# Kernel optimization log

Measured on AMD Instinct MI355X. Metric: run time of the kernel, lower is better.

## Reference

```python
import jax, jax.numpy as jnp
import numpy as np

B, N, E, H, HEADS = 4, 10000, 160000, 128, 4
NEG_SLOPE = 0.2  # PyG GATConv default
LN_EPS = 1e-5


def setup_inputs() -> dict:
    key = jax.random.key(0)
    ks = jax.random.split(key, 24)
    inp = {}
    inp["node_embeddings"] = jax.random.normal(ks[0], (B, N, H), dtype=jnp.float32)
    inp["src_index"] = jax.random.randint(ks[1], (B, E), 0, N)
    inp["tgt_index"] = jax.random.randint(ks[2], (B, E), 0, N)
    sc = 1.0 / np.sqrt(H)
    for i in range(3):
        j = 3 + 3 * i
        inp[f"W{i+1}"] = jax.random.normal(ks[j], (H, HEADS * H), dtype=jnp.float32) * sc
        inp[f"att_src{i+1}"] = jax.random.normal(ks[j + 1], (HEADS, H), dtype=jnp.float32) * sc
        inp[f"att_dst{i+1}"] = jax.random.normal(ks[j + 2], (HEADS, H), dtype=jnp.float32) * sc
        inp[f"bias{i+1}"] = jnp.zeros((H,), dtype=jnp.float32)
    inp["ln1_g"] = jnp.ones((H,), dtype=jnp.float32)
    inp["ln1_b"] = jnp.zeros((H,), dtype=jnp.float32)
    inp["ln2_g"] = jnp.ones((H,), dtype=jnp.float32)
    inp["ln2_b"] = jnp.zeros((H,), dtype=jnp.float32)
    return inp


def _layer_norm(x, g, b):
    mu = jnp.mean(x, axis=-1, keepdims=True)
    var = jnp.mean((x - mu) ** 2, axis=-1, keepdims=True)
    return (x - mu) * jax.lax.rsqrt(var + LN_EPS) * g + b


def _gat(x, src, tgt, W, a_s, a_d, b):
    # x: [N, H]; src/tgt: [E'] (self-loops already appended). eval mode -> no dropout.
    h = (x @ W).reshape(N, HEADS, H)               # [N, heads, H]
    e_src = jnp.einsum('nhc,hc->nh', h, a_s)       # [N, heads]
    e_dst = jnp.einsum('nhc,hc->nh', h, a_d)
    e = jax.nn.leaky_relu(e_src[src] + e_dst[tgt], NEG_SLOPE)  # [E', heads]
    m = jax.ops.segment_max(e, tgt, num_segments=N)            # per-target max
    ex = jnp.exp(e - m[tgt])
    s = jax.ops.segment_sum(ex, tgt, num_segments=N)
    alpha = ex / s[tgt]                                        # [E', heads]
    out = jax.ops.segment_sum(alpha[:, :, None] * h[src], tgt, num_segments=N)
    return out.mean(axis=1) + b                                # concat=False -> head mean


def reference(node_embeddings, src_index, tgt_index,
              W1, att_src1, att_dst1, bias1,
              W2, att_src2, att_dst2, bias2,
              W3, att_src3, att_dst3, bias3,
              ln1_g, ln1_b, ln2_g, ln2_b):
    loop = jnp.arange(N, dtype=src_index.dtype)

    def one_graph(x, src, tgt):
        s = jnp.concatenate([src, loop])   # GATConv add_self_loops=True (default)
        t = jnp.concatenate([tgt, loop])
        m = _gat(x, s, t, W1, att_src1, att_dst1, bias1)
        m = jax.nn.relu(_layer_norm(m, ln1_g, ln1_b))
        m = _gat(m, s, t, W2, att_src2, att_dst2, bias2)
        m = jax.nn.relu(_layer_norm(m, ln2_g, ln2_b))
        m = _gat(m, s, t, W3, att_src3, att_dst3, bias3)
        return m

    return jax.vmap(one_graph)(node_embeddings, src_index, tgt_index)
```

## Files before the change

kernel.cpp:

```cpp
#include <hip/hip_runtime.h>
#include <hip/hip_bf16.h>
#include <cstdint>
#include <cstddef>

#define B_ 4
#define N_ 10000
#define E_ 160000
#define H_ 128
#define HEADS_ 4
#define HH_ 512
#define NROWS (B_*N_)

typedef __attribute__((ext_vector_type(8))) short bf16x8;
typedef __attribute__((ext_vector_type(4))) float f32x4;

__device__ __forceinline__ float lrelu(float x){ return x > 0.f ? x : 0.2f*x; }
__device__ __forceinline__ unsigned short f2b(float f){
  unsigned int u = __builtin_bit_cast(unsigned int, f);
  unsigned int r = (u + 0x7fffu + ((u >> 16) & 1u)) >> 16;
  return (unsigned short)r;
}
__device__ __forceinline__ float blo(unsigned int u){ return __builtin_bit_cast(float, u << 16); }
__device__ __forceinline__ float bhi(unsigned int u){ return __builtin_bit_cast(float, u & 0xffff0000u); }

__global__ void k_count(const int* __restrict__ tgt, int* __restrict__ cnt){
  int e = blockIdx.x*blockDim.x + threadIdx.x;
  int b = blockIdx.y;
  int t = tgt[(size_t)b*E_ + e];
  atomicAdd(&cnt[b*N_ + t], 1);
}

__global__ void k_scan(const int* __restrict__ cnt, int* __restrict__ off, int* __restrict__ cursor){
  int b = blockIdx.x;
  __shared__ int wsum[16];
  __shared__ int carry_s;
  int lane = threadIdx.x & 63, wid = threadIdx.x >> 6;
  if (threadIdx.x == 0){ carry_s = 0; off[b*(N_+1)] = 0; }
  __syncthreads();
  for (int base = 0; base < N_; base += 1024){
    int i = base + threadIdx.x;
    int v = (i < N_) ? cnt[b*N_ + i] : 0;
    int x = v;
    #pragma unroll
    for (int d = 1; d < 64; d <<= 1){
      int y = __shfl_up(x, d);
      if (lane >= d) x += y;
    }
    if (lane == 63) wsum[wid] = x;
    __syncthreads();
    if (wid == 0 && lane < 16){
      int w = wsum[lane];
      #pragma unroll
      for (int d = 1; d < 16; d <<= 1){
        int y = __shfl_up(w, d, 16);
        if (lane >= d) w += y;
      }
      wsum[lane] = w;
    }
    __syncthreads();
    int excl = (wid ? wsum[wid-1] : 0) + carry_s;
    if (i < N_){
      int inc = x + excl;
      off[b*(N_+1) + i + 1] = inc;
      cursor[b*N_ + i] = inc - v;
    }
    __syncthreads();
    if (threadIdx.x == 0) carry_s += wsum[15];
    __syncthreads();
  }
}

__global__ void k_scatter(const int* __restrict__ src, const int* __restrict__ tgt,
                          int* __restrict__ cursor, int* __restrict__ csr){
  int e = blockIdx.x*blockDim.x + threadIdx.x;
  int b = blockIdx.y;
  int t = tgt[(size_t)b*E_ + e];
  int pos = atomicAdd(&cursor[b*N_ + t], 1);
  csr[(size_t)b*E_ + pos] = src[(size_t)b*E_ + e];
}

__global__ void k_wa(const float* __restrict__ W, const float* __restrict__ as_,
                     const float* __restrict__ ad_, float* __restrict__ was, float* __restrict__ wad){
  int i = blockIdx.x*blockDim.x + threadIdx.x;
  if (i >= H_*HEADS_) return;
  int k = i >> 2, h = i & 3;
  const float* wrow = W + (size_t)k*HH_ + h*H_;
  const float* asr = as_ + h*H_;
  const float* adr = ad_ + h*H_;
  float ss = 0.f, sd = 0.f;
  for (int c = 0; c < H_; ++c){ float w = wrow[c]; ss += w*asr[c]; sd += w*adr[c]; }
  was[i] = ss; wad[i] = sd;
}

__global__ void k_wprep(const float* __restrict__ W, unsigned short* __restrict__ Wt){
  int i = blockIdx.x*blockDim.x + threadIdx.x;
  int c = i >> 7, k = i & 127;
  Wt[i] = f2b(W[(size_t)k*HH_ + c]);
}

__global__ __launch_bounds__(256) void k_cast(const float* __restrict__ X, unsigned short* __restrict__ Xb){
  int i = blockIdx.x*blockDim.x + threadIdx.x;
  float4 v = ((const float4*)X)[i];
  ushort4 o; o.x = f2b(v.x); o.y = f2b(v.y); o.z = f2b(v.z); o.w = f2b(v.w);
  ((ushort4*)Xb)[i] = o;
}

__global__ __launch_bounds__(256) void k_logits(const unsigned short* __restrict__ Xb,
    const float* __restrict__ was, const float* __restrict__ wad,
    float* __restrict__ es, float* __restrict__ ed){
  int gw = (blockIdx.x * blockDim.x + threadIdx.x) >> 6;
  int lane = threadIdx.x & 63;
  unsigned int u = *(const unsigned int*)(Xb + (size_t)gw*H_ + lane*2);
  float xlo = blo(u), xhi = bhi(u);
  float4 w0 = *(const float4*)(was + lane*8);
  float4 w1 = *(const float4*)(was + lane*8 + 4);
  float4 d0 = *(const float4*)(wad + lane*8);
  float4 d1 = *(const float4*)(wad + lane*8 + 4);
  float s0 = xlo*w0.x + xhi*w1.x;
  float s1 = xlo*w0.y + xhi*w1.y;
  float s2 = xlo*w0.z + xhi*w1.z;
  float s3 = xlo*w0.w + xhi*w1.w;
  float t0 = xlo*d0.x + xhi*d1.x;
  float t1 = xlo*d0.y + xhi*d1.y;
  float t2 = xlo*d0.z + xhi*d1.z;
  float t3 = xlo*d0.w + xhi*d1.w;
  #pragma unroll
  for (int d = 1; d < 64; d <<= 1){
    s0 += __shfl_xor(s0, d); s1 += __shfl_xor(s1, d);
    s2 += __shfl_xor(s2, d); s3 += __shfl_xor(s3, d);
    t0 += __shfl_xor(t0, d); t1 += __shfl_xor(t1, d);
    t2 += __shfl_xor(t2, d); t3 += __shfl_xor(t3, d);
  }
  if (lane == 0){
    *(float4*)(es + (size_t)gw*4) = make_float4(s0, s1, s2, s3);
    *(float4*)(ed + (size_t)gw*4) = make_float4(t0, t1, t2, t3);
  }
}

__global__ __launch_bounds__(256) void k_gemm_mfma(const unsigned short* __restrict__ Xb,
    const unsigned short* __restrict__ Wt, unsigned short* __restrict__ Hb){
  __shared__ unsigned short xs[64*128];
  __shared__ unsigned short ws[64*128];
  int row0 = blockIdx.x * 64, col0 = blockIdx.y * 64;
  int tid = threadIdx.x;
  int ch = tid & 15, r0 = tid >> 4;
  #pragma unroll
  for (int p = 0; p < 4; ++p){
    int r = r0 + p*16;
    int sc = ch ^ (r & 7);
    *(uint4*)(&xs[r*128 + sc*8]) = *(const uint4*)(Xb + (size_t)(row0 + r)*H_ + ch*8);
    *(uint4*)(&ws[r*128 + sc*8]) = *(const uint4*)(Wt + (size_t)(col0 + r)*H_ + ch*8);
  }
  __syncthreads();
  int w = tid >> 6, l = tid & 63;
  int lr = l & 15, q = l >> 4;
  f32x4 z = {0.f, 0.f, 0.f, 0.f};
  f32x4 acc[4] = {z, z, z, z};
  int arow = w*16 + lr;
  #pragma unroll
  for (int kf = 0; kf < 4; ++kf){
    int bch = kf*4 + q;
    bf16x8 a = *(const bf16x8*)(&xs[arow*128 + (bch ^ (arow & 7))*8]);
    #pragma unroll
    for (int cf = 0; cf < 4; ++cf){
      int brow = cf*16 + lr;
      bf16x8 bfr = *(const bf16x8*)(&ws[brow*128 + (bch ^ (brow & 7))*8]);
      acc[cf] = __builtin_amdgcn_mfma_f32_16x16x32_bf16(a, bfr, acc[cf], 0, 0, 0);
    }
  }
  #pragma unroll
  for (int cf = 0; cf < 4; ++cf){
    #pragma unroll
    for (int rg = 0; rg < 4; ++rg){
      int row = row0 + w*16 + q*4 + rg;
      int col = col0 + cf*16 + lr;
      Hb[(size_t)row*HH_ + col] = f2b(acc[cf][rg]);
    }
  }
}

__global__ __launch_bounds__(256) void k_aggregate(const unsigned short* __restrict__ Hb,
    const float* __restrict__ es, const float* __restrict__ ed,
    const int* __restrict__ off, const int* __restrict__ csr,
    const float* __restrict__ bias, float* __restrict__ Y){
  int gw = (blockIdx.x * blockDim.x + threadIdx.x) >> 6;
  int lane = threadIdx.x & 63;
  int b = gw / N_;
  int t = gw - b*N_;
  const float4 edv = *(const float4*)(ed + (size_t)gw*4);
  int start = off[b*(N_+1) + t];
  int deg = off[b*(N_+1) + t + 1] - start;
  const int* lst = csr + (size_t)b*E_ + start;

  float m0=-1e30f, m1=-1e30f, m2=-1e30f, m3=-1e30f;
  float s0=0.f, s1=0.f, s2=0.f, s3=0.f;
  for (int i = lane; i <= deg; i += 64){
    int srcn = (i < deg) ? lst[i] : t;
    float4 ev = *(const float4*)(es + (size_t)(b*N_ + srcn)*4);
    float e0 = lrelu(ev.x + edv.x);
    float e1 = lrelu(ev.y + edv.y);
    float e2 = lrelu(ev.z + edv.z);
    float e3 = lrelu(ev.w + edv.w);
    float nm;
    nm = fmaxf(m0, e0); s0 = s0*__expf(m0-nm) + __expf(e0-nm); m0 = nm;
    nm = fmaxf(m1, e1); s1 = s1*__expf(m1-nm) + __expf(e1-nm); m1 = nm;
    nm = fmaxf(m2, e2); s2 = s2*__expf(m2-nm) + __expf(e2-nm); m2 = nm;
    nm = fmaxf(m3, e3); s3 = s3*__expf(m3-nm) + __expf(e3-nm); m3 = nm;
  }
  #pragma unroll
  for (int d = 1; d < 64; d <<= 1){
    float om, os, nm;
    om = __shfl_xor(m0, d); os = __shfl_xor(s0, d); nm = fmaxf(m0, om);
    s0 = s0*__expf(m0-nm) + os*__expf(om-nm); m0 = nm;
    om = __shfl_xor(m1, d); os = __shfl_xor(s1, d); nm = fmaxf(m1, om);
    s1 = s1*__expf(m1-nm) + os*__expf(om-nm); m1 = nm;
    om = __shfl_xor(m2, d); os = __shfl_xor(s2, d); nm = fmaxf(m2, om);
    s2 = s2*__expf(m2-nm) + os*__expf(om-nm); m2 = nm;
    om = __shfl_xor(m3, d); os = __shfl_xor(s3, d); nm = fmaxf(m3, om);
    s3 = s3*__expf(m3-nm) + os*__expf(om-nm); m3 = nm;
  }

  int head = lane >> 4;
  float mh, sh, edh;
  if      (head == 0){ mh = m0; sh = s0; edh = edv.x; }
  else if (head == 1){ mh = m1; sh = s1; edh = edv.y; }
  else if (head == 2){ mh = m2; sh = s2; edh = edv.z; }
  else               { mh = m3; sh = s3; edh = edv.w; }
  float rh = 1.0f / sh;
  int cb = head*H_ + (lane & 15)*8;
  const unsigned short* hbase = Hb + (size_t)b*N_*HH_;
  const float* esb = es + (size_t)b*N_*4;
  float a[8] = {0.f,0.f,0.f,0.f,0.f,0.f,0.f,0.f};
  int total = deg + 1;
  int i = 0;
  for (; i + 1 < total; i += 2){
    int sA = lst[i];
    int sB = (i + 1 < deg) ? lst[i+1] : t;
    float eA = esb[(size_t)sA*4 + head];
    float eB = esb[(size_t)sB*4 + head];
    uint4 hA = *(const uint4*)(hbase + (size_t)sA*HH_ + cb);
    uint4 hB = *(const uint4*)(hbase + (size_t)sB*HH_ + cb);
    float aA = __expf(lrelu(eA + edh) - mh) * rh;
    float aB = __expf(lrelu(eB + edh) - mh) * rh;
    a[0] += aA*blo(hA.x); a[1] += aA*bhi(hA.x);
    a[2] += aA*blo(hA.y); a[3] += aA*bhi(hA.y);
    a[4] += aA*blo(hA.z); a[5] += aA*bhi(hA.z);
    a[6] += aA*blo(hA.w); a[7] += aA*bhi(hA.w);
    a[0] += aB*blo(hB.x); a[1] += aB*bhi(hB.x);
    a[2] += aB*blo(hB.y); a[3] += aB*bhi(hB.y);
    a[4] += aB*blo(hB.z); a[5] += aB*bhi(hB.z);
    a[6] += aB*blo(hB.w); a[7] += aB*bhi(hB.w);
  }
  if (i < total){
    int sA = (i < deg) ? lst[i] : t;
    float eA = esb[(size_t)sA*4 + head];
    uint4 hA = *(const uint4*)(hbase + (size_t)sA*HH_ + cb);
    float aA = __expf(lrelu(eA + edh) - mh) * rh;
    a[0] += aA*blo(hA.x); a[1] += aA*bhi(hA.x);
    a[2] += aA*blo(hA.y); a[3] += aA*bhi(hA.y);
    a[4] += aA*blo(hA.z); a[5] += aA*bhi(hA.z);
    a[6] += aA*blo(hA.w); a[7] += aA*bhi(hA.w);
  }
  #pragma unroll
  for (int d = 16; d < 64; d <<= 1)
    #pragma unroll
    for (int j = 0; j < 8; j++) a[j] += __shfl_xor(a[j], d);
  if (lane < 16){
    int c = lane*8;
    float4 o0 = make_float4(0.25f*a[0]+bias[c+0], 0.25f*a[1]+bias[c+1],
                            0.25f*a[2]+bias[c+2], 0.25f*a[3]+bias[c+3]);
    float4 o1 = make_float4(0.25f*a[4]+bias[c+4], 0.25f*a[5]+bias[c+5],
                            0.25f*a[6]+bias[c+6], 0.25f*a[7]+bias[c+7]);
    *(float4*)(Y + (size_t)gw*H_ + c)     = o0;
    *(float4*)(Y + (size_t)gw*H_ + c + 4) = o1;
  }
}

__global__ __launch_bounds__(256) void k_lnrelu(const float* __restrict__ Y,
    const float* __restrict__ g, const float* __restrict__ bb, unsigned short* __restrict__ Xb){
  int gw = (blockIdx.x*blockDim.x + threadIdx.x) >> 6;
  int lane = threadIdx.x & 63;
  float2 v = *(const float2*)(Y + (size_t)gw*H_ + lane*2);
  float sum = v.x + v.y;
  #pragma unroll
  for (int d = 1; d < 64; d <<= 1) sum += __shfl_xor(sum, d);
  float mu = sum * (1.f/H_);
  float dx = v.x - mu, dy = v.y - mu;
  float vs = dx*dx + dy*dy;
  #pragma unroll
  for (int d = 1; d < 64; d <<= 1) vs += __shfl_xor(vs, d);
  float inv = rsqrtf(vs*(1.f/H_) + 1e-5f);
  float2 gv = *(const float2*)(g + lane*2);
  float2 bv = *(const float2*)(bb + lane*2);
  float ox = fmaxf(dx*inv*gv.x + bv.x, 0.f);
  float oy = fmaxf(dy*inv*gv.y + bv.y, 0.f);
  unsigned int o = ((unsigned int)f2b(oy) << 16) | (unsigned int)f2b(ox);
  *(unsigned int*)(Xb + (size_t)gw*H_ + lane*2) = o;
}

extern "C" void kernel_launch(void* const* d_in, const int* in_sizes, int n_in,
                              void* d_out, int out_size, void* d_ws, size_t ws_size,
                              hipStream_t stream){
  const float* x0   = (const float*)d_in[0];
  const int*   srcI = (const int*)d_in[1];
  const int*   tgtI = (const int*)d_in[2];
  const float* Wl[3]  = {(const float*)d_in[3], (const float*)d_in[7],  (const float*)d_in[11]};
  const float* asl[3] = {(const float*)d_in[4], (const float*)d_in[8],  (const float*)d_in[12]};
  const float* adl[3] = {(const float*)d_in[5], (const float*)d_in[9],  (const float*)d_in[13]};
  const float* bl[3]  = {(const float*)d_in[6], (const float*)d_in[10], (const float*)d_in[14]};
  const float* lng[2] = {(const float*)d_in[15], (const float*)d_in[17]};
  const float* lnb[2] = {(const float*)d_in[16], (const float*)d_in[18]};

  char* p = (char*)d_ws;
  auto carve = [&](size_t bytes) -> void* {
    void* r = (void*)p; p += (bytes + 255) & ~(size_t)255; return r;
  };
  int*   off    = (int*)carve((size_t)B_*(N_+1)*4);
  int*   cnt    = (int*)carve((size_t)B_*N_*4);
  int*   cursor = (int*)carve((size_t)B_*N_*4);
  int*   csr    = (int*)carve((size_t)B_*E_*4);
  float* es     = (float*)carve((size_t)B_*N_*HEADS_*4);
  float* ed     = (float*)carve((size_t)B_*N_*HEADS_*4);
  float* was    = (float*)carve((size_t)H_*HEADS_*4);
  float* wad    = (float*)carve((size_t)H_*HEADS_*4);
  unsigned short* hbuf = (unsigned short*)carve((size_t)NROWS*HH_*2);
  unsigned short* xbf  = (unsigned short*)carve((size_t)NROWS*H_*2);
  unsigned short* wtb  = (unsigned short*)carve((size_t)HH_*H_*2);
  float* tbuf   = (float*)carve((size_t)NROWS*H_*4);

  hipMemsetAsync(cnt, 0, (size_t)B_*N_*4, stream);
  k_count  <<<dim3(E_/256, B_), 256, 0, stream>>>(tgtI, cnt);
  k_scan   <<<B_, 1024, 0, stream>>>(cnt, off, cursor);
  k_scatter<<<dim3(E_/256, B_), 256, 0, stream>>>(srcI, tgtI, cursor, csr);
  k_cast   <<<NROWS*H_/4/256, 256, 0, stream>>>(x0, xbf);

  for (int l = 0; l < 3; ++l){
    k_wa    <<<2, 256, 0, stream>>>(Wl[l], asl[l], adl[l], was, wad);
    k_wprep <<<HH_*H_/256, 256, 0, stream>>>(Wl[l], wtb);
    k_logits<<<NROWS/4, 256, 0, stream>>>(xbf, was, wad, es, ed);
    k_gemm_mfma<<<dim3(NROWS/64, HH_/64), 256, 0, stream>>>(xbf, wtb, hbuf);
    float* yout = (l == 2) ? (float*)d_out : tbuf;
    k_aggregate<<<NROWS/4, 256, 0, stream>>>(hbuf, es, ed, off, csr, bl[l], yout);
    if (l < 2){
      k_lnrelu<<<NROWS/4, 256, 0, stream>>>(tbuf, lng[l], lnb[l], xbf);
    }
  }
}
```

Baseline: 518.2 us.

## Fuse LayerNorm, ReLU and next-layer logits into aggregation; batch weight prep

Moves the weight transpose and attention-vector projection for all three layers into one prep kernel, and merges the fp32-to-bf16 cast with the first logits computation. The aggregation kernel now applies bias, LayerNorm and ReLU in its epilogue, writes bf16 features and the next layer's attention logits directly, and uses ping-pong logit buffers. This removes the fp32 intermediate round-trip and several small launches per layer. It also adds a fast path for nodes with at most 64 incoming edges that computes alpha once into shared memory instead of recomputing exp per channel group, at the cost of more registers and shared memory per block.

```diff
diff --git a/kernel.cpp b/kernel.cpp
--- a/kernel.cpp
+++ b/kernel.cpp
@@ -13,6 +13,7 @@
 
 typedef __attribute__((ext_vector_type(8))) short bf16x8;
 typedef __attribute__((ext_vector_type(4))) float f32x4;
+typedef __attribute__((ext_vector_type(2))) float f32x2;
 
 __device__ __forceinline__ float lrelu(float x){ return x > 0.f ? x : 0.2f*x; }
 __device__ __forceinline__ unsigned short f2b(float f){
@@ -79,61 +80,55 @@
   csr[(size_t)b*E_ + pos] = src[(size_t)b*E_ + e];
 }
 
-__global__ void k_wa(const float* __restrict__ W, const float* __restrict__ as_,
-                     const float* __restrict__ ad_, float* __restrict__ was, float* __restrict__ wad){
-  int i = blockIdx.x*blockDim.x + threadIdx.x;
-  if (i >= H_*HEADS_) return;
-  int k = i >> 2, h = i & 3;
-  const float* wrow = W + (size_t)k*HH_ + h*H_;
-  const float* asr = as_ + h*H_;
-  const float* adr = ad_ + h*H_;
-  float ss = 0.f, sd = 0.f;
-  for (int c = 0; c < H_; ++c){ float w = wrow[c]; ss += w*asr[c]; sd += w*adr[c]; }
-  was[i] = ss; wad[i] = sd;
-}
-
-__global__ void k_wprep(const float* __restrict__ W, unsigned short* __restrict__ Wt){
-  int i = blockIdx.x*blockDim.x + threadIdx.x;
-  int c = i >> 7, k = i & 127;
-  Wt[i] = f2b(W[(size_t)k*HH_ + c]);
-}
-
-__global__ __launch_bounds__(256) void k_cast(const float* __restrict__ X, unsigned short* __restrict__ Xb){
-  int i = blockIdx.x*blockDim.x + threadIdx.x;
-  float4 v = ((const float4*)X)[i];
-  ushort4 o; o.x = f2b(v.x); o.y = f2b(v.y); o.z = f2b(v.z); o.w = f2b(v.w);
-  ((ushort4*)Xb)[i] = o;
-}
-
-__global__ __launch_bounds__(256) void k_logits(const unsigned short* __restrict__ Xb,
+__global__ void k_prep(const float* __restrict__ W0, const float* __restrict__ W1, const float* __restrict__ W2,
+                       const float* __restrict__ as0, const float* __restrict__ as1, const float* __restrict__ as2,
+                       const float* __restrict__ ad0, const float* __restrict__ ad1, const float* __restrict__ ad2,
+                       float* __restrict__ wasA, float* __restrict__ wadA, unsigned short* __restrict__ wtA){
+  int l = blockIdx.y;
+  const float* W   = (l==0)?W0:(l==1)?W1:W2;
+  const float* asp = (l==0)?as0:(l==1)?as1:as2;
+  const float* adp = (l==0)?ad0:(l==1)?ad1:ad2;
+  if (blockIdx.x < 256){
+    int i = blockIdx.x*256 + threadIdx.x;
+    int c = i >> 7, k = i & 127;
+    wtA[(size_t)l*HH_*H_ + i] = f2b(W[(size_t)k*HH_ + c]);
+  } else {
+    int j = (blockIdx.x - 256)*256 + threadIdx.x;
+    if (j < H_*HEADS_){
+      int k = j >> 2, h = j & 3;
+      const float* wrow = W + (size_t)k*HH_ + h*H_;
+      const float* asr = asp + h*H_;
+      const float* adr = adp + h*H_;
+      float ss = 0.f, sd = 0.f;
+      for (int c = 0; c < H_; ++c){ float w = wrow[c]; ss += w*asr[c]; sd += w*adr[c]; }
+      wasA[l*HH_ + j] = ss; wadA[l*HH_ + j] = sd;
+    }
+  }
+}
+
+__global__ __launch_bounds__(256) void k_cast_logits(const float* __restrict__ X,
     const float* __restrict__ was, const float* __restrict__ wad,
-    float* __restrict__ es, float* __restrict__ ed){
-  int gw = (blockIdx.x * blockDim.x + threadIdx.x) >> 6;
+    unsigned short* __restrict__ Xb, float* __restrict__ es, float* __restrict__ ed){
+  int gw = (blockIdx.x*blockDim.x + threadIdx.x) >> 6;
   int lane = threadIdx.x & 63;
-  unsigned int u = *(const unsigned int*)(Xb + (size_t)gw*H_ + lane*2);
-  float xlo = blo(u), xhi = bhi(u);
-  float4 w0 = *(const float4*)(was + lane*8);
-  float4 w1 = *(const float4*)(was + lane*8 + 4);
-  float4 d0 = *(const float4*)(wad + lane*8);
-  float4 d1 = *(const float4*)(wad + lane*8 + 4);
-  float s0 = xlo*w0.x + xhi*w1.x;
-  float s1 = xlo*w0.y + xhi*w1.y;
-  float s2 = xlo*w0.z + xhi*w1.z;
-  float s3 = xlo*w0.w + xhi*w1.w;
-  float t0 = xlo*d0.x + xhi*d1.x;
-  float t1 = xlo*d0.y + xhi*d1.y;
-  float t2 = xlo*d0.z + xhi*d1.z;
-  float t3 = xlo*d0.w + xhi*d1.w;
+  float2 v = *(const float2*)(X + (size_t)gw*H_ + lane*2);
+  unsigned int o = ((unsigned int)f2b(v.y) << 16) | (unsigned int)f2b(v.x);
+  *(unsigned int*)(Xb + (size_t)gw*H_ + lane*2) = o;
+  int c = lane*2;
+  const f32x4* w4 = (const f32x4*)was;
+  const f32x4* d4 = (const f32x4*)wad;
+  f32x4 se = v.x*w4[c] + v.y*w4[c+1];
+  f32x4 de = v.x*d4[c] + v.y*d4[c+1];
   #pragma unroll
   for (int d = 1; d < 64; d <<= 1){
-    s0 += __shfl_xor(s0, d); s1 += __shfl_xor(s1, d);
-    s2 += __shfl_xor(s2, d); s3 += __shfl_xor(s3, d);
-    t0 += __shfl_xor(t0, d); t1 += __shfl_xor(t1, d);
-    t2 += __shfl_xor(t2, d); t3 += __shfl_xor(t3, d);
+    se.x += __shfl_xor(se.x,d); se.y += __shfl_xor(se.y,d);
+    se.z += __shfl_xor(se.z,d); se.w += __shfl_xor(se.w,d);
+    de.x += __shfl_xor(de.x,d); de.y += __shfl_xor(de.y,d);
+    de.z += __shfl_xor(de.z,d); de.w += __shfl_xor(de.w,d);
   }
   if (lane == 0){
-    *(float4*)(es + (size_t)gw*4) = make_float4(s0, s1, s2, s3);
-    *(float4*)(ed + (size_t)gw*4) = make_float4(t0, t1, t2, t3);
+    *(float4*)(es + (size_t)gw*4) = make_float4(se.x, se.y, se.z, se.w);
+    *(float4*)(ed + (size_t)gw*4) = make_float4(de.x, de.y, de.z, de.w);
   }
 }
 
@@ -179,123 +174,202 @@
   }
 }
 
-__global__ __launch_bounds__(256) void k_aggregate(const unsigned short* __restrict__ Hb,
+template<bool FINAL>
+__global__ __launch_bounds__(256) void k_aggregate(
+    const unsigned short* __restrict__ Hb,
     const float* __restrict__ es, const float* __restrict__ ed,
     const int* __restrict__ off, const int* __restrict__ csr,
-    const float* __restrict__ bias, float* __restrict__ Y){
-  int gw = (blockIdx.x * blockDim.x + threadIdx.x) >> 6;
-  int lane = threadIdx.x & 63;
-  int b = gw / N_;
-  int t = gw - b*N_;
+    const float* __restrict__ bias,
+    const float* __restrict__ wasN, const float* __restrict__ wadN,
+    const float* __restrict__ lng, const float* __restrict__ lnb,
+    float* __restrict__ Yout, unsigned short* __restrict__ Xbout,
+    float* __restrict__ esN, float* __restrict__ edN)
+{
+  __shared__ float alpha_s[4][64][4];
+  __shared__ int   srcn_s[4][64];
+  __shared__ float orow_s[4][128];
+  int wv = threadIdx.x >> 6, lane = threadIdx.x & 63;
+  int gw = blockIdx.x*4 + wv;
+  int b = gw / N_, t = gw - b*N_;
   const float4 edv = *(const float4*)(ed + (size_t)gw*4);
   int start = off[b*(N_+1) + t];
   int deg = off[b*(N_+1) + t + 1] - start;
+  int total = deg + 1;
   const int* lst = csr + (size_t)b*E_ + start;
-
-  float m0=-1e30f, m1=-1e30f, m2=-1e30f, m3=-1e30f;
-  float s0=0.f, s1=0.f, s2=0.f, s3=0.f;
-  for (int i = lane; i <= deg; i += 64){
-    int srcn = (i < deg) ? lst[i] : t;
-    float4 ev = *(const float4*)(es + (size_t)(b*N_ + srcn)*4);
-    float e0 = lrelu(ev.x + edv.x);
-    float e1 = lrelu(ev.y + edv.y);
-    float e2 = lrelu(ev.z + edv.z);
-    float e3 = lrelu(ev.w + edv.w);
-    float nm;
-    nm = fmaxf(m0, e0); s0 = s0*__expf(m0-nm) + __expf(e0-nm); m0 = nm;
-    nm = fmaxf(m1, e1); s1 = s1*__expf(m1-nm) + __expf(e1-nm); m1 = nm;
-    nm = fmaxf(m2, e2); s2 = s2*__expf(m2-nm) + __expf(e2-nm); m2 = nm;
-    nm = fmaxf(m3, e3); s3 = s3*__expf(m3-nm) + __expf(e3-nm); m3 = nm;
-  }
-  #pragma unroll
-  for (int d = 1; d < 64; d <<= 1){
-    float om, os, nm;
-    om = __shfl_xor(m0, d); os = __shfl_xor(s0, d); nm = fmaxf(m0, om);
-    s0 = s0*__expf(m0-nm) + os*__expf(om-nm); m0 = nm;
-    om = __shfl_xor(m1, d); os = __shfl_xor(s1, d); nm = fmaxf(m1, om);
-    s1 = s1*__expf(m1-nm) + os*__expf(om-nm); m1 = nm;
-    om = __shfl_xor(m2, d); os = __shfl_xor(s2, d); nm = fmaxf(m2, om);
-    s2 = s2*__expf(m2-nm) + os*__expf(om-nm); m2 = nm;
-    om = __shfl_xor(m3, d); os = __shfl_xor(s3, d); nm = fmaxf(m3, om);
-    s3 = s3*__expf(m3-nm) + os*__expf(om-nm); m3 = nm;
-  }
-
+  const float* esb = es + (size_t)b*N_*4;
   int head = lane >> 4;
-  float mh, sh, edh;
-  if      (head == 0){ mh = m0; sh = s0; edh = edv.x; }
-  else if (head == 1){ mh = m1; sh = s1; edh = edv.y; }
-  else if (head == 2){ mh = m2; sh = s2; edh = edv.z; }
-  else               { mh = m3; sh = s3; edh = edv.w; }
-  float rh = 1.0f / sh;
   int cb = head*H_ + (lane & 15)*8;
   const unsigned short* hbase = Hb + (size_t)b*N_*HH_;
-  const float* esb = es + (size_t)b*N_*4;
-  float a[8] = {0.f,0.f,0.f,0.f,0.f,0.f,0.f,0.f};
-  int total = deg + 1;
-  int i = 0;
-  for (; i + 1 < total; i += 2){
-    int sA = lst[i];
-    int sB = (i + 1 < deg) ? lst[i+1] : t;
-    float eA = esb[(size_t)sA*4 + head];
-    float eB = esb[(size_t)sB*4 + head];
-    uint4 hA = *(const uint4*)(hbase + (size_t)sA*HH_ + cb);
-    uint4 hB = *(const uint4*)(hbase + (size_t)sB*HH_ + cb);
-    float aA = __expf(lrelu(eA + edh) - mh) * rh;
-    float aB = __expf(lrelu(eB + edh) - mh) * rh;
-    a[0] += aA*blo(hA.x); a[1] += aA*bhi(hA.x);
-    a[2] += aA*blo(hA.y); a[3] += aA*bhi(hA.y);
-    a[4] += aA*blo(hA.z); a[5] += aA*bhi(hA.z);
-    a[6] += aA*blo(hA.w); a[7] += aA*bhi(hA.w);
-    a[0] += aB*blo(hB.x); a[1] += aB*bhi(hB.x);
-    a[2] += aB*blo(hB.y); a[3] += aB*bhi(hB.y);
-    a[4] += aB*blo(hB.z); a[5] += aB*bhi(hB.z);
-    a[6] += aB*blo(hB.w); a[7] += aB*bhi(hB.w);
-  }
-  if (i < total){
-    int sA = (i < deg) ? lst[i] : t;
-    float eA = esb[(size_t)sA*4 + head];
-    uint4 hA = *(const uint4*)(hbase + (size_t)sA*HH_ + cb);
-    float aA = __expf(lrelu(eA + edh) - mh) * rh;
-    a[0] += aA*blo(hA.x); a[1] += aA*bhi(hA.x);
-    a[2] += aA*blo(hA.y); a[3] += aA*bhi(hA.y);
-    a[4] += aA*blo(hA.z); a[5] += aA*bhi(hA.z);
-    a[6] += aA*blo(hA.w); a[7] += aA*bhi(hA.w);
-  }
+  f32x2 zz = {0.f, 0.f};
+  f32x2 ac[4] = {zz, zz, zz, zz};
+
+  if (total <= 64){
+    bool valid = lane < total;
+    int srcn = (lane < deg) ? lst[lane] : t;
+    srcn_s[wv][lane] = srcn;
+    float4 ev = *(const float4*)(esb + (size_t)srcn*4);
+    float e0 = valid ? lrelu(ev.x + edv.x) : -1e30f;
+    float e1 = valid ? lrelu(ev.y + edv.y) : -1e30f;
+    float e2 = valid ? lrelu(ev.z + edv.z) : -1e30f;
+    float e3 = valid ? lrelu(ev.w + edv.w) : -1e30f;
+    float M0 = e0, M1 = e1, M2 = e2, M3 = e3;
+    #pragma unroll
+    for (int d = 1; d < 64; d <<= 1){
+      M0 = fmaxf(M0, __shfl_xor(M0, d)); M1 = fmaxf(M1, __shfl_xor(M1, d));
+      M2 = fmaxf(M2, __shfl_xor(M2, d)); M3 = fmaxf(M3, __shfl_xor(M3, d));
+    }
+    float p0 = valid ? __expf(e0 - M0) : 0.f;
+    float p1 = valid ? __expf(e1 - M1) : 0.f;
+    float p2 = valid ? __expf(e2 - M2) : 0.f;
+    float p3 = valid ? __expf(e3 - M3) : 0.f;
+    float S0 = p0, S1 = p1, S2 = p2, S3 = p3;
+    #pragma unroll
+    for (int d = 1; d < 64; d <<= 1){
+      S0 += __shfl_xor(S0, d); S1 += __shfl_xor(S1, d);
+      S2 += __shfl_xor(S2, d); S3 += __shfl_xor(S3, d);
+    }
+    *(float4*)(&alpha_s[wv][lane][0]) = make_float4(p0/S0, p1/S1, p2/S2, p3/S3);
+    __builtin_amdgcn_wave_barrier();
+
+    int i = 0;
+    for (; i + 2 <= total; i += 2){
+      int sA = srcn_s[wv][i];
+      int sB = srcn_s[wv][i+1];
+      float aA = alpha_s[wv][i][head];
+      float aB = alpha_s[wv][i+1][head];
+      uint4 hA = *(const uint4*)(hbase + (size_t)sA*HH_ + cb);
+      uint4 hB = *(const uint4*)(hbase + (size_t)sB*HH_ + cb);
+      f32x2 vA = {aA, aA}, vB = {aB, aB};
+      ac[0] += vA * (f32x2){blo(hA.x), bhi(hA.x)};
+      ac[1] += vA * (f32x2){blo(hA.y), bhi(hA.y)};
+      ac[2] += vA * (f32x2){blo(hA.z), bhi(hA.z)};
+      ac[3] += vA * (f32x2){blo(hA.w), bhi(hA.w)};
+      ac[0] += vB * (f32x2){blo(hB.x), bhi(hB.x)};
+      ac[1] += vB * (f32x2){blo(hB.y), bhi(hB.y)};
+      ac[2] += vB * (f32x2){blo(hB.z), bhi(hB.z)};
+      ac[3] += vB * (f32x2){blo(hB.w), bhi(hB.w)};
+    }
+    if (i < total){
+      int sA = srcn_s[wv][i];
+      float aA = alpha_s[wv][i][head];
+      uint4 hA = *(const uint4*)(hbase + (size_t)sA*HH_ + cb);
+      f32x2 vA = {aA, aA};
+      ac[0] += vA * (f32x2){blo(hA.x), bhi(hA.x)};
+      ac[1] += vA * (f32x2){blo(hA.y), bhi(hA.y)};
+      ac[2] += vA * (f32x2){blo(hA.z), bhi(hA.z)};
+      ac[3] += vA * (f32x2){blo(hA.w), bhi(hA.w)};
+    }
+  } else {
+    float m0=-1e30f, m1=-1e30f, m2=-1e30f, m3=-1e30f;
+    float s0=0.f, s1=0.f, s2=0.f, s3=0.f;
+    for (int i2 = lane; i2 <= deg; i2 += 64){
+      int srcn = (i2 < deg) ? lst[i2] : t;
+      float4 ev = *(const float4*)(esb + (size_t)srcn*4);
+      float e0 = lrelu(ev.x + edv.x);
+      float e1 = lrelu(ev.y + edv.y);
+      float e2 = lrelu(ev.z + edv.z);
+      float e3 = lrelu(ev.w + edv.w);
+      float nm;
+      nm = fmaxf(m0, e0); s0 = s0*__expf(m0-nm) + __expf(e0-nm); m0 = nm;
+      nm = fmaxf(m1, e1); s1 = s1*__expf(m1-nm) + __expf(e1-nm); m1 = nm;
+      nm = fmaxf(m2, e2); s2 = s2*__expf(m2-nm) + __expf(e2-nm); m2 = nm;
+      nm = fmaxf(m3, e3); s3 = s3*__expf(m3-nm) + __expf(e3-nm); m3 = nm;
+    }
+    #pragma unroll
+    for (int d = 1; d < 64; d <<= 1){
+      float om, os, nm;
+      om = __shfl_xor(m0, d); os = __shfl_xor(s0, d); nm = fmaxf(m0, om);
+      s0 = s0*__expf(m0-nm) + os*__expf(om-nm); m0 = nm;
+      om = __shfl_xor(m1, d); os = __shfl_xor(s1, d); nm = fmaxf(m1, om);
+      s1 = s1*__expf(m1-nm) + os*__expf(om-nm); m1 = nm;
+      om = __shfl_xor(m2, d); os = __shfl_xor(s2, d); nm = fmaxf(m2, om);
+      s2 = s2*__expf(m2-nm) + os*__expf(om-nm); m2 = nm;
+      om = __shfl_xor(m3, d); os = __shfl_xor(s3, d); nm = fmaxf(m3, om);
+      s3 = s3*__expf(m3-nm) + os*__expf(om-nm); m3 = nm;
+    }
+    float mh, sh, edh;
+    if      (head == 0){ mh = m0; sh = s0; edh = edv.x; }
+    else if (head == 1){ mh = m1; sh = s1; edh = edv.y; }
+    else if (head == 2){ mh = m2; sh = s2; edh = edv.z; }
+    else               { mh = m3; sh = s3; edh = edv.w; }
+    float rh = 1.0f / sh;
+    for (int i2 = 0; i2 < total; ++i2){
+      int srcn = (i2 < deg) ? lst[i2] : t;
+      float eh = esb[(size_t)srcn*4 + head];
+      float al = __expf(lrelu(eh + edh) - mh) * rh;
+      uint4 hA = *(const uint4*)(hbase + (size_t)srcn*HH_ + cb);
+      f32x2 vA = {al, al};
+      ac[0] += vA * (f32x2){blo(hA.x), bhi(hA.x)};
+      ac[1] += vA * (f32x2){blo(hA.y), bhi(hA.y)};
+      ac[2] += vA * (f32x2){blo(hA.z), bhi(hA.z)};
+      ac[3] += vA * (f32x2){blo(hA.w), bhi(hA.w)};
+    }
+  }
+
+  float a[8] = {ac[0].x, ac[0].y, ac[1].x, ac[1].y, ac[2].x, ac[2].y, ac[3].x, ac[3].y};
   #pragma unroll
   for (int d = 16; d < 64; d <<= 1)
     #pragma unroll
     for (int j = 0; j < 8; j++) a[j] += __shfl_xor(a[j], d);
-  if (lane < 16){
-    int c = lane*8;
-    float4 o0 = make_float4(0.25f*a[0]+bias[c+0], 0.25f*a[1]+bias[c+1],
-                            0.25f*a[2]+bias[c+2], 0.25f*a[3]+bias[c+3]);
-    float4 o1 = make_float4(0.25f*a[4]+bias[c+4], 0.25f*a[5]+bias[c+5],
-                            0.25f*a[6]+bias[c+6], 0.25f*a[7]+bias[c+7]);
-    *(float4*)(Y + (size_t)gw*H_ + c)     = o0;
-    *(float4*)(Y + (size_t)gw*H_ + c + 4) = o1;
-  }
-}
-
-__global__ __launch_bounds__(256) void k_lnrelu(const float* __restrict__ Y,
-    const float* __restrict__ g, const float* __restrict__ bb, unsigned short* __restrict__ Xb){
-  int gw = (blockIdx.x*blockDim.x + threadIdx.x) >> 6;
-  int lane = threadIdx.x & 63;
-  float2 v = *(const float2*)(Y + (size_t)gw*H_ + lane*2);
-  float sum = v.x + v.y;
-  #pragma unroll
-  for (int d = 1; d < 64; d <<= 1) sum += __shfl_xor(sum, d);
-  float mu = sum * (1.f/H_);
-  float dx = v.x - mu, dy = v.y - mu;
-  float vs = dx*dx + dy*dy;
-  #pragma unroll
-  for (int d = 1; d < 64; d <<= 1) vs += __shfl_xor(vs, d);
-  float inv = rsqrtf(vs*(1.f/H_) + 1e-5f);
-  float2 gv = *(const float2*)(g + lane*2);
-  float2 bv = *(const float2*)(bb + lane*2);
-  float ox = fmaxf(dx*inv*gv.x + bv.x, 0.f);
-  float oy = fmaxf(dy*inv*gv.y + bv.y, 0.f);
-  unsigned int o = ((unsigned int)f2b(oy) << 16) | (unsigned int)f2b(ox);
-  *(unsigned int*)(Xb + (size_t)gw*H_ + lane*2) = o;
+
+  int c = (lane & 15)*8;
+  if (FINAL){
+    if (lane < 16){
+      float4 o0 = make_float4(0.25f*a[0]+bias[c+0], 0.25f*a[1]+bias[c+1],
+                              0.25f*a[2]+bias[c+2], 0.25f*a[3]+bias[c+3]);
+      float4 o1 = make_float4(0.25f*a[4]+bias[c+4], 0.25f*a[5]+bias[c+5],
+                              0.25f*a[6]+bias[c+6], 0.25f*a[7]+bias[c+7]);
+      *(float4*)(Yout + (size_t)gw*H_ + c)     = o0;
+      *(float4*)(Yout + (size_t)gw*H_ + c + 4) = o1;
+    }
+  } else {
+    float o[8];
+    #pragma unroll
+    for (int j = 0; j < 8; j++) o[j] = 0.25f*a[j] + bias[c+j];
+    float ss = 0.f;
+    #pragma unroll
+    for (int j = 0; j < 8; j++) ss += o[j];
+    #pragma unroll
+    for (int d = 1; d < 16; d <<= 1) ss += __shfl_xor(ss, d);
+    float mu = ss * (1.f/H_);
+    float vv = 0.f;
+    #pragma unroll
+    for (int j = 0; j < 8; j++){ float dx = o[j]-mu; vv += dx*dx; }
+    #pragma unroll
+    for (int d = 1; d < 16; d <<= 1) vv += __shfl_xor(vv, d);
+    float inv = rsqrtf(vv*(1.f/H_) + 1e-5f);
+    float4 g0 = *(const float4*)(lng + c), g1 = *(const float4*)(lng + c + 4);
+    float4 b0 = *(const float4*)(lnb + c), b1 = *(const float4*)(lnb + c + 4);
+    float gg[8] = {g0.x,g0.y,g0.z,g0.w,g1.x,g1.y,g1.z,g1.w};
+    float bb[8] = {b0.x,b0.y,b0.z,b0.w,b1.x,b1.y,b1.z,b1.w};
+    float oo[8];
+    #pragma unroll
+    for (int j = 0; j < 8; j++) oo[j] = fmaxf((o[j]-mu)*inv*gg[j] + bb[j], 0.f);
+    if (lane < 16){
+      uint4 up;
+      up.x = ((unsigned int)f2b(oo[1]) << 16) | f2b(oo[0]);
+      up.y = ((unsigned int)f2b(oo[3]) << 16) | f2b(oo[2]);
+      up.z = ((unsigned int)f2b(oo[5]) << 16) | f2b(oo[4]);
+      up.w = ((unsigned int)f2b(oo[7]) << 16) | f2b(oo[6]);
+      *(uint4*)(Xbout + (size_t)gw*H_ + lane*8) = up;
+      *(float4*)(&orow_s[wv][c])     = make_float4(oo[0], oo[1], oo[2], oo[3]);
+      *(float4*)(&orow_s[wv][c + 4]) = make_float4(oo[4], oo[5], oo[6], oo[7]);
+    }
+    __builtin_amdgcn_wave_barrier();
+    float pe = 0.f, pd = 0.f;
+    #pragma unroll
+    for (int j = 0; j < 8; j++){
+      float xv = orow_s[wv][c + j];
+      pe += xv * wasN[(c + j)*4 + head];
+      pd += xv * wadN[(c + j)*4 + head];
+    }
+    #pragma unroll
+    for (int d = 1; d < 16; d <<= 1){ pe += __shfl_xor(pe, d); pd += __shfl_xor(pd, d); }
+    if ((lane & 15) == 0){
+      esN[(size_t)gw*4 + head] = pe;
+      edN[(size_t)gw*4 + head] = pd;
+    }
+  }
 }
 
 extern "C" void kernel_launch(void* const* d_in, const int* in_sizes, int n_in,
@@ -319,30 +393,35 @@
   int*   cnt    = (int*)carve((size_t)B_*N_*4);
   int*   cursor = (int*)carve((size_t)B_*N_*4);
   int*   csr    = (int*)carve((size_t)B_*E_*4);
-  float* es     = (float*)carve((size_t)B_*N_*HEADS_*4);
-  float* ed     = (float*)carve((size_t)B_*N_*HEADS_*4);
-  float* was    = (float*)carve((size_t)H_*HEADS_*4);
-  float* wad    = (float*)carve((size_t)H_*HEADS_*4);
+  float* es2[2] = {(float*)carve((size_t)NROWS*4*4), (float*)carve((size_t)NROWS*4*4)};
+  float* ed2[2] = {(float*)carve((size_t)NROWS*4*4), (float*)carve((size_t)NROWS*4*4)};
+  float* wasA   = (float*)carve((size_t)3*HH_*4);
+  float* wadA   = (float*)carve((size_t)3*HH_*4);
+  unsigned short* wtA  = (unsigned short*)carve((size_t)3*HH_*H_*2);
   unsigned short* hbuf = (unsigned short*)carve((size_t)NROWS*HH_*2);
   unsigned short* xbf  = (unsigned short*)carve((size_t)NROWS*H_*2);
-  unsigned short* wtb  = (unsigned short*)carve((size_t)HH_*H_*2);
-  float* tbuf   = (float*)carve((size_t)NROWS*H_*4);
 
   hipMemsetAsync(cnt, 0, (size_t)B_*N_*4, stream);
   k_count  <<<dim3(E_/256, B_), 256, 0, stream>>>(tgtI, cnt);
   k_scan   <<<B_, 1024, 0, stream>>>(cnt, off, cursor);
   k_scatter<<<dim3(E_/256, B_), 256, 0, stream>>>(srcI, tgtI, cursor, csr);
-  k_cast   <<<NROWS*H_/4/256, 256, 0, stream>>>(x0, xbf);
+  k_prep   <<<dim3(258, 3), 256, 0, stream>>>(Wl[0], Wl[1], Wl[2],
+                                              asl[0], asl[1], asl[2],
+                                              adl[0], adl[1], adl[2],
+                                              wasA, wadA, wtA);
+  k_cast_logits<<<NROWS/4, 256, 0, stream>>>(x0, wasA, wadA, xbf, es2[0], ed2[0]);
 
   for (int l = 0; l < 3; ++l){
-    k_wa    <<<2, 256, 0, stream>>>(Wl[l], asl[l], adl[l], was, wad);
-    k_wprep <<<HH_*H_/256, 256, 0, stream>>>(Wl[l], wtb);
-    k_logits<<<NROWS/4, 256, 0, stream>>>(xbf, was, wad, es, ed);
-    k_gemm_mfma<<<dim3(NROWS/64, HH_/64), 256, 0, stream>>>(xbf, wtb, hbuf);
-    float* yout = (l == 2) ? (float*)d_out : tbuf;
-    k_aggregate<<<NROWS/4, 256, 0, stream>>>(hbuf, es, ed, off, csr, bl[l], yout);
+    k_gemm_mfma<<<dim3(NROWS/64, HH_/64), 256, 0, stream>>>(xbf, wtA + (size_t)l*HH_*H_, hbuf);
+    int cur = l & 1, nxt = cur ^ 1;
     if (l < 2){
-      k_lnrelu<<<NROWS/4, 256, 0, stream>>>(tbuf, lng[l], lnb[l], xbf);
-    }
-  }
-}
+      k_aggregate<false><<<NROWS/4, 256, 0, stream>>>(hbuf, es2[cur], ed2[cur], off, csr, bl[l],
+          wasA + (size_t)(l+1)*HH_, wadA + (size_t)(l+1)*HH_, lng[l], lnb[l],
+          nullptr, xbf, es2[nxt], ed2[nxt]);
+    } else {
+      k_aggregate<true><<<NROWS/4, 256, 0, stream>>>(hbuf, es2[cur], ed2[cur], off, csr, bl[l],
+          nullptr, nullptr, nullptr, nullptr,
+          (float*)d_out, nullptr, nullptr, nullptr);
+    }
+  }
+}
```

Result: faster. 488.6 us (-5.7%).
